# Performance work log

Measured on AMD Instinct MI355X. Metric: run time of the kernel, lower is better.

## Reference

```python
import jax, jax.numpy as jnp
import numpy as np

N_X, N_U, N_Y = 256, 32, 32
BATCH, T = 16, 8192
LAM_MIN, LAM_MAX = 0.9, 0.995
B_SCALE, D_SCALE = 0.25, 0.25


def setup_inputs() -> dict:
    key = jax.random.key(0)
    k = jax.random.split(key, 6)
    # Orthogonal Q via QR of a random Gaussian matrix (as in the torch module)
    M = jax.random.normal(k[0], (N_X, N_X), dtype=jnp.float32)
    Q, _ = jnp.linalg.qr(M)
    lam = LAM_MIN + (LAM_MAX - LAM_MIN) * jax.random.uniform(k[1], (N_X,), dtype=jnp.float32)
    Bmat = B_SCALE * jax.random.normal(k[2], (N_X, N_U), dtype=jnp.float32)
    # C picks out the first n_y coordinates (C[i, i] = 1)
    C = jnp.eye(N_Y, N_X, dtype=jnp.float32)
    D = D_SCALE * jax.random.normal(k[3], (N_Y, N_U), dtype=jnp.float32)
    x0 = jax.random.normal(k[4], (BATCH, N_X), dtype=jnp.float32)
    u = jax.random.normal(k[5], (BATCH, T, N_U), dtype=jnp.float32)
    return {"x0": x0, "u": u, "Q": Q, "lam": lam, "Bmat": Bmat, "C": C, "D": D}


def _diag_scan(lam, v):
    """Diagonal linear recurrence x_t = lam * x_{t-1} + v_t (x_0 folded into v[:, 0]).

    lam: (N,), v: (B, T, N) -> states x_1..x_T of shape (B, T, N).
    """
    a = jnp.broadcast_to(lam, v.shape)

    def op(l, r):
        a1, b1 = l
        a2, b2 = r
        return a1 * a2, a2 * b1 + b2

    return jax.lax.associative_scan(op, (a, v), axis=1)[1]


def reference(x0, u, Q, lam, Bmat, C, D):
    Bz = Q.T @ Bmat            # (n_x, n_u) modal input matrix
    Cz = C @ Q                 # (n_y, n_x) modal output matrix
    z0 = x0 @ Q                # (B, n_x)   modal initial state
    v = jnp.einsum('btu,nu->btn', u, Bz)   # (B, T, n_x)
    v = v.at[:, 0].add(lam * z0)            # fold lam * z0 into first step
    z_next = _diag_scan(lam, v)             # (B, T, n_x) = z_1..z_T
    # y_t uses z_t for t = 0..T-1 (states[:, :-1] in the original)
    z_prev = jnp.concatenate([z0[:, None, :], z_next[:, :-1]], axis=1)
    y = jnp.einsum('btn,yn->bty', z_prev, Cz) + jnp.einsum('btu,yu->bty', u, D)
    return y
```

## Files before the change

### kernel.cpp

```cpp
#include <hip/hip_runtime.h>

typedef _Float16 half4_t __attribute__((ext_vector_type(4)));
typedef _Float16 half8_t __attribute__((ext_vector_type(8)));
typedef float f32x4 __attribute__((ext_vector_type(4)));

constexpr int NX = 256, NU = 32, NY = 32, BATCH = 16, T = 8192;
constexpr int NC = 64, L = 128;
constexpr int SUBT = 32, NSUB = L / SUBT;
constexpr int ZP = 264;

__global__ __launch_bounds__(256) void k_pre(
    const float* __restrict__ x0, const float* __restrict__ Q,
    const float* __restrict__ Bm,
    _Float16* __restrict__ Bzh, float* __restrict__ z0)
{
    int o = blockIdx.x * 64 + (threadIdx.x >> 2);
    int p = threadIdx.x & 3;
    if (o >= 12288) return;
    float s = 0.f;
    int k0 = p * 64;
    if (o < 8192) {
        int n = o >> 5, j = o & 31;
        for (int k = k0; k < k0 + 64; ++k) s = fmaf(Q[k * NX + n], Bm[k * NU + j], s);
    } else {
        int g = o - 8192; int b = g >> 8, nn = g & 255;
        for (int k = k0; k < k0 + 64; ++k) s = fmaf(x0[b * NX + k], Q[k * NX + nn], s);
    }
    s += __shfl_xor(s, 1);
    s += __shfl_xor(s, 2);
    if (p == 0) {
        if (o < 8192) Bzh[o] = (_Float16)s;
        else          z0[o - 8192] = s;
    }
}

__global__ __launch_bounds__(256) void k_phase1(
    const float* __restrict__ u, const float* __restrict__ lam,
    const _Float16* __restrict__ Bzh, float* __restrict__ S)
{
    __shared__ __align__(16) _Float16 ut[2][SUBT][32];

    const int b = blockIdx.x >> 6, c = blockIdx.x & 63, tid = threadIdx.x;
    const int w = tid >> 6, lane = tid & 63, m16 = lane & 15, quad = lane >> 4;
    const int rot = (m16 & 3) * 8;
    const int tr = tid >> 3, cb = ((tid & 7) * 4 + (tr & 3) * 8) & 31;

    const float* ug = u + ((size_t)(b * T) + (size_t)c * L) * NU;
    float4 ucur = *(const float4*)(ug + tid * 4);

    half8_t bfrag[4];
    #pragma unroll
    for (int i = 0; i < 4; ++i)
        bfrag[i] = *(const half8_t*)&Bzh[((4 * w + i) * 16 + m16) * NU + quad * 8];

    float wr[4][4], wt16[4], l32[4], acc[4];
    #pragma unroll
    for (int i = 0; i < 4; ++i) {
        float la = lam[(4 * w + i) * 16 + m16];
        float p2 = la * la, p4 = p2 * p2, p8 = p4 * p4, p16 = p8 * p8;
        float inv1 = 1.0f / la;
        float inv4 = (inv1 * inv1) * (inv1 * inv1);
        float pq = 1.0f;
        if (quad & 1) pq *= inv4;
        if (quad & 2) pq *= inv4 * inv4;
        float w0 = (p16 * p8 * p4 * p2 * la) * pq;
        wr[i][0] = w0;
        wr[i][1] = w0 * inv1;
        wr[i][2] = wr[i][1] * inv1;
        wr[i][3] = wr[i][2] * inv1;
        wt16[i] = 1.0f / p16;
        l32[i] = p16 * p16;
        acc[i] = 0.f;
    }

    {
        half4_t h; h.x = (_Float16)ucur.x; h.y = (_Float16)ucur.y;
        h.z = (_Float16)ucur.z; h.w = (_Float16)ucur.w;
        *(half4_t*)&ut[0][tr][cb] = h;
    }
    __syncthreads();
    float4 unext = *(const float4*)(ug + (size_t)SUBT * NU + tid * 4);

    for (int sub = 0; sub < NSUB; ++sub) {
        half8_t af0 = *(const half8_t*)&ut[sub & 1][m16][(quad * 8 + rot) & 31];
        half8_t af1 = *(const half8_t*)&ut[sub & 1][16 + m16][(quad * 8 + rot) & 31];
        if (sub < NSUB - 2)
            ucur = *(const float4*)(ug + (size_t)(sub + 2) * SUBT * NU + tid * 4);
        #pragma unroll
        for (int i = 0; i < 4; ++i) {
            f32x4 z4 = {0.f, 0.f, 0.f, 0.f};
            f32x4 v0 = __builtin_amdgcn_mfma_f32_16x16x32_f16(af0, bfrag[i], z4, 0, 0, 0);
            f32x4 v1 = __builtin_amdgcn_mfma_f32_16x16x32_f16(af1, bfrag[i], z4, 0, 0, 0);
            float s0 = wr[i][0] * v0[0] + wr[i][1] * v0[1] + wr[i][2] * v0[2] + wr[i][3] * v0[3];
            float s1 = wr[i][0] * v1[0] + wr[i][1] * v1[1] + wr[i][2] * v1[2] + wr[i][3] * v1[3];
            acc[i] = fmaf(l32[i], acc[i], fmaf(wt16[i], s1, s0));
        }
        if (sub < NSUB - 1) {
            half4_t h; h.x = (_Float16)unext.x; h.y = (_Float16)unext.y;
            h.z = (_Float16)unext.z; h.w = (_Float16)unext.w;
            *(half4_t*)&ut[(sub + 1) & 1][tr][cb] = h;
            unext = ucur;
            __syncthreads();
        }
    }
    #pragma unroll
    for (int i = 0; i < 4; ++i) {
        acc[i] += __shfl_xor(acc[i], 16);
        acc[i] += __shfl_xor(acc[i], 32);
    }
    float out = quad == 0 ? acc[0] : quad == 1 ? acc[1] : quad == 2 ? acc[2] : acc[3];
    S[(size_t)blockIdx.x * NX + (4 * w + quad) * 16 + m16] = out;
}

__global__ __launch_bounds__(256) void k_phase3(
    const float* __restrict__ u, const float* __restrict__ lam,
    const _Float16* __restrict__ Bzh, const float* __restrict__ Q,
    const float* __restrict__ D, const float* __restrict__ S,
    const float* __restrict__ z0, float* __restrict__ y)
{
    __shared__ __align__(16) _Float16 ut[2][SUBT][32];
    __shared__ __align__(16) _Float16 zt[2][SUBT][ZP];
    __shared__ float pvec[NX];

    const int b = blockIdx.x >> 6, c = blockIdx.x & 63, tid = threadIdx.x;
    const int w = tid >> 6, lane = tid & 63, m16 = lane & 15, quad = lane >> 4;
    const int tw = w & 1, yw = w >> 1;
    const int rot = (m16 & 3) * 8;
    const int tr = tid >> 3, cb = ((tid & 7) * 4 + (tr & 3) * 8) & 31;

    const float* ug = u + ((size_t)(b * T) + (size_t)c * L) * NU;
    float4 ucur = *(const float4*)(ug + tid * 4);

    {
        float la = lam[tid];
        float l2L = 128.0f * __log2f(la);
        const float* Sb = S + (size_t)(b * NC) * NX + tid;
        float pv = 0.f;
        #pragma unroll 8
        for (int k = 0; k < c; ++k) {
            float wgt = exp2f((float)k * l2L);
            pv = fmaf(wgt, Sb[(size_t)(c - 1 - k) * NX], pv);
        }
        pvec[tid] = fmaf(exp2f((float)c * l2L), z0[b * NX + tid], pv);
    }

    half8_t bfrag[4];
    #pragma unroll
    for (int i = 0; i < 4; ++i)
        bfrag[i] = *(const half8_t*)&Bzh[((4 * w + i) * 16 + m16) * NU + quad * 8];
    half8_t wfrag[9];
    #pragma unroll
    for (int kk = 0; kk < 8; ++kk) {
        float4 qa = *(const float4*)&Q[(size_t)(yw * 16 + m16) * NX + kk * 32 + quad * 8];
        float4 qb = *(const float4*)&Q[(size_t)(yw * 16 + m16) * NX + kk * 32 + quad * 8 + 4];
        half8_t hh;
        hh[0] = (_Float16)qa.x; hh[1] = (_Float16)qa.y; hh[2] = (_Float16)qa.z; hh[3] = (_Float16)qa.w;
        hh[4] = (_Float16)qb.x; hh[5] = (_Float16)qb.y; hh[6] = (_Float16)qb.z; hh[7] = (_Float16)qb.w;
        wfrag[kk] = hh;
    }
    {
        float4 da = *(const float4*)&D[(size_t)(yw * 16 + m16) * NU + quad * 8];
        float4 db = *(const float4*)&D[(size_t)(yw * 16 + m16) * NU + quad * 8 + 4];
        half8_t hh;
        hh[0] = (_Float16)da.x; hh[1] = (_Float16)da.y; hh[2] = (_Float16)da.z; hh[3] = (_Float16)da.w;
        hh[4] = (_Float16)db.x; hh[5] = (_Float16)db.y; hh[6] = (_Float16)db.z; hh[7] = (_Float16)db.w;
        wfrag[8] = hh;
    }

    float lamn[4], inv1[4], iq[4], i16p[4], fq[4], f16p[4], l32[4], p[4];
    #pragma unroll
    for (int i = 0; i < 4; ++i) {
        int ni = (4 * w + i) * 16 + m16;
        float la = lam[ni];
        lamn[i] = la;
        float p2 = la * la, p4 = p2 * p2, p8 = p4 * p4, p16 = p8 * p8;
        float iv = 1.0f / la;
        inv1[i] = iv;
        float iv4 = (iv * iv) * (iv * iv);
        float pqi = 1.0f, pqf = 1.0f;
        if (quad & 1) { pqi *= iv4; pqf *= p4; }
        if (quad & 2) { pqi *= iv4 * iv4; pqf *= p8; }
        iq[i] = iv * pqi;
        fq[i] = pqf;
        i16p[i] = 1.0f / p16;
        f16p[i] = p16;
        l32[i] = p16 * p16;
    }

    {
        half4_t h; h.x = (_Float16)ucur.x; h.y = (_Float16)ucur.y;
        h.z = (_Float16)ucur.z; h.w = (_Float16)ucur.w;
        *(half4_t*)&ut[0][tr][cb] = h;
    }
    __syncthreads();
    #pragma unroll
    for (int i = 0; i < 4; ++i)
        p[i] = pvec[(4 * w + i) * 16 + m16];
    float4 unext = *(const float4*)(ug + (size_t)SUBT * NU + tid * 4);

    float* yg = y + ((size_t)(b * T) + (size_t)c * L) * NY;

    for (int sub = 0; sub < NSUB; ++sub) {
        half8_t af0 = *(const half8_t*)&ut[sub & 1][m16][(quad * 8 + rot) & 31];
        half8_t af1 = *(const half8_t*)&ut[sub & 1][16 + m16][(quad * 8 + rot) & 31];
        if (sub < NSUB - 2)
            ucur = *(const float4*)(ug + (size_t)(sub + 2) * SUBT * NU + tid * 4);
        #pragma unroll
        for (int i = 0; i < 4; ++i) {
            int ni = (4 * w + i) * 16 + m16;
            f32x4 z4 = {0.f, 0.f, 0.f, 0.f};
            f32x4 v0 = __builtin_amdgcn_mfma_f32_16x16x32_f16(af0, bfrag[i], z4, 0, 0, 0);
            f32x4 v1 = __builtin_amdgcn_mfma_f32_16x16x32_f16(af1, bfrag[i], z4, 0, 0, 0);
            float a0[4], a1[4];
            float sc = iq[i];
            #pragma unroll
            for (int r = 0; r < 4; ++r) {
                a0[r] = v0[r] * sc;
                a1[r] = v1[r] * (sc * i16p[i]);
                sc *= inv1[i];
            }
            float e0[4], e1[4];
            e0[0] = 0.f; e0[1] = a0[0]; e0[2] = e0[1] + a0[1]; e0[3] = e0[2] + a0[2];
            float S40 = e0[3] + a0[3];
            e1[0] = 0.f; e1[1] = a1[0]; e1[2] = e1[1] + a1[1]; e1[3] = e1[2] + a1[2];
            float S41 = e1[3] + a1[3];
            float incl0 = S40;
            float t0 = __shfl_up(incl0, 16); if (quad >= 1) incl0 += t0;
            t0 = __shfl_up(incl0, 32);       if (quad >= 2) incl0 += t0;
            float excl0 = incl0 - S40;
            float total0 = __shfl(incl0, 48 + m16);
            float incl1 = S41;
            float t1 = __shfl_up(incl1, 16); if (quad >= 1) incl1 += t1;
            t1 = __shfl_up(incl1, 32);       if (quad >= 2) incl1 += t1;
            float excl1 = incl1 - S41;
            float total1 = __shfl(incl1, 48 + m16);
            float f = fq[i];
            #pragma unroll
            for (int r = 0; r < 4; ++r) {
                float zv0 = f * (p[i] + (excl0 + e0[r]));
                float zv1 = (f * f16p[i]) * (p[i] + (total0 + excl1 + e1[r]));
                zt[sub & 1][quad * 4 + r][ni] = (_Float16)zv0;
                zt[sub & 1][16 + quad * 4 + r][ni] = (_Float16)zv1;
                f *= lamn[i];
            }
            p[i] = l32[i] * (p[i] + (total0 + total1));
        }
        if (sub < NSUB - 1) {
            half4_t h; h.x = (_Float16)unext.x; h.y = (_Float16)unext.y;
            h.z = (_Float16)unext.z; h.w = (_Float16)unext.w;
            *(half4_t*)&ut[(sub + 1) & 1][tr][cb] = h;
            unext = ucur;
        }
        __syncthreads();

        f32x4 acc = {0.f, 0.f, 0.f, 0.f};
        #pragma unroll
        for (int kk = 0; kk < 8; ++kk) {
            half8_t az = *(const half8_t*)&zt[sub & 1][tw * 16 + m16][kk * 32 + quad * 8];
            acc = __builtin_amdgcn_mfma_f32_16x16x32_f16(wfrag[kk], az, acc, 0, 0, 0);
        }
        {
            half8_t au = tw ? af1 : af0;
            acc = __builtin_amdgcn_mfma_f32_16x16x32_f16(wfrag[8], au, acc, 0, 0, 0);
        }
        {
            float4 v = make_float4(acc[0], acc[1], acc[2], acc[3]);
            *(float4*)&yg[(size_t)(sub * SUBT + tw * 16 + m16) * NY + yw * 16 + quad * 4] = v;
        }
    }
}

extern "C" void kernel_launch(void* const* d_in, const int* in_sizes, int n_in,
                              void* d_out, int out_size, void* d_ws, size_t ws_size,
                              hipStream_t stream) {
    (void)in_sizes; (void)n_in; (void)out_size; (void)ws_size;
    const float* x0  = (const float*)d_in[0];
    const float* u   = (const float*)d_in[1];
    const float* Q   = (const float*)d_in[2];
    const float* lam = (const float*)d_in[3];
    const float* Bm  = (const float*)d_in[4];
    const float* D   = (const float*)d_in[6];
    float* y = (float*)d_out;

    char* ws = (char*)d_ws;
    _Float16* Bzh = (_Float16*)(ws);
    float*    z0  = (float*)(ws + 16384);
    float*    S   = (float*)(ws + 32768);

    k_pre   <<<192, 256, 0, stream>>>(x0, Q, Bm, Bzh, z0);
    k_phase1<<<BATCH * NC, 256, 0, stream>>>(u, lam, Bzh, S);
    k_phase3<<<BATCH * NC, 256, 0, stream>>>(u, lam, Bzh, Q, D, S, z0, y);
}
```

Before: 118.4 us.

## Load MFMA input fragments directly from global memory, drop LDS staging of u

Each lane now reads its own u fragment rows from global memory, with a one-step register prefetch, and converts them to fp16 in registers. This replaces the cooperative load into LDS, the fp16 stores and the barrier per sub-tile. In phase3 the z tile goes from double buffering to a single buffer, with an extra barrier after the output MFMA to protect it, which cuts LDS use. In exchange, the u rows are read redundantly by every wave (4x in each block), and global loads are less coalesced than the earlier one-float4-per-thread pattern.

New measurement: 129.7 us. 9.5% more time.

```diff
diff --git a/kernel.cpp b/kernel.cpp
--- a/kernel.cpp
+++ b/kernel.cpp
@@ -8,6 +8,13 @@
 constexpr int NC = 64, L = 128;
 constexpr int SUBT = 32, NSUB = L / SUBT;
 constexpr int ZP = 264;
+
+__device__ __forceinline__ half8_t cvt8(float4 a, float4 b) {
+    half8_t h;
+    h[0] = (_Float16)a.x; h[1] = (_Float16)a.y; h[2] = (_Float16)a.z; h[3] = (_Float16)a.w;
+    h[4] = (_Float16)b.x; h[5] = (_Float16)b.y; h[6] = (_Float16)b.z; h[7] = (_Float16)b.w;
+    return h;
+}
 
 __global__ __launch_bounds__(256) void k_pre(
     const float* __restrict__ x0, const float* __restrict__ Q,
@@ -38,15 +45,15 @@
     const float* __restrict__ u, const float* __restrict__ lam,
     const _Float16* __restrict__ Bzh, float* __restrict__ S)
 {
-    __shared__ __align__(16) _Float16 ut[2][SUBT][32];
-
     const int b = blockIdx.x >> 6, c = blockIdx.x & 63, tid = threadIdx.x;
     const int w = tid >> 6, lane = tid & 63, m16 = lane & 15, quad = lane >> 4;
-    const int rot = (m16 & 3) * 8;
-    const int tr = tid >> 3, cb = ((tid & 7) * 4 + (tr & 3) * 8) & 31;
 
     const float* ug = u + ((size_t)(b * T) + (size_t)c * L) * NU;
-    float4 ucur = *(const float4*)(ug + tid * 4);
+    const float* r0 = ug + (size_t)m16 * NU + quad * 8;
+    const float* r1 = ug + (size_t)(16 + m16) * NU + quad * 8;
+
+    float4 c0a = *(const float4*)r0, c0b = *(const float4*)(r0 + 4);
+    float4 c1a = *(const float4*)r1, c1b = *(const float4*)(r1 + 4);
 
     half8_t bfrag[4];
     #pragma unroll
@@ -73,19 +80,15 @@
         acc[i] = 0.f;
     }
 
-    {
-        half4_t h; h.x = (_Float16)ucur.x; h.y = (_Float16)ucur.y;
-        h.z = (_Float16)ucur.z; h.w = (_Float16)ucur.w;
-        *(half4_t*)&ut[0][tr][cb] = h;
-    }
-    __syncthreads();
-    float4 unext = *(const float4*)(ug + (size_t)SUBT * NU + tid * 4);
-
     for (int sub = 0; sub < NSUB; ++sub) {
-        half8_t af0 = *(const half8_t*)&ut[sub & 1][m16][(quad * 8 + rot) & 31];
-        half8_t af1 = *(const half8_t*)&ut[sub & 1][16 + m16][(quad * 8 + rot) & 31];
-        if (sub < NSUB - 2)
-            ucur = *(const float4*)(ug + (size_t)(sub + 2) * SUBT * NU + tid * 4);
+        half8_t af0 = cvt8(c0a, c0b);
+        half8_t af1 = cvt8(c1a, c1b);
+        if (sub < NSUB - 1) {
+            const float* n0 = r0 + (size_t)(sub + 1) * SUBT * NU;
+            const float* n1 = r1 + (size_t)(sub + 1) * SUBT * NU;
+            c0a = *(const float4*)n0; c0b = *(const float4*)(n0 + 4);
+            c1a = *(const float4*)n1; c1b = *(const float4*)(n1 + 4);
+        }
         #pragma unroll
         for (int i = 0; i < 4; ++i) {
             f32x4 z4 = {0.f, 0.f, 0.f, 0.f};
@@ -95,13 +98,6 @@
             float s1 = wr[i][0] * v1[0] + wr[i][1] * v1[1] + wr[i][2] * v1[2] + wr[i][3] * v1[3];
             acc[i] = fmaf(l32[i], acc[i], fmaf(wt16[i], s1, s0));
         }
-        if (sub < NSUB - 1) {
-            half4_t h; h.x = (_Float16)unext.x; h.y = (_Float16)unext.y;
-            h.z = (_Float16)unext.z; h.w = (_Float16)unext.w;
-            *(half4_t*)&ut[(sub + 1) & 1][tr][cb] = h;
-            unext = ucur;
-            __syncthreads();
-        }
     }
     #pragma unroll
     for (int i = 0; i < 4; ++i) {
@@ -118,18 +114,19 @@
     const float* __restrict__ D, const float* __restrict__ S,
     const float* __restrict__ z0, float* __restrict__ y)
 {
-    __shared__ __align__(16) _Float16 ut[2][SUBT][32];
-    __shared__ __align__(16) _Float16 zt[2][SUBT][ZP];
+    __shared__ __align__(16) _Float16 zt[SUBT][ZP];
     __shared__ float pvec[NX];
 
     const int b = blockIdx.x >> 6, c = blockIdx.x & 63, tid = threadIdx.x;
     const int w = tid >> 6, lane = tid & 63, m16 = lane & 15, quad = lane >> 4;
     const int tw = w & 1, yw = w >> 1;
-    const int rot = (m16 & 3) * 8;
-    const int tr = tid >> 3, cb = ((tid & 7) * 4 + (tr & 3) * 8) & 31;
 
     const float* ug = u + ((size_t)(b * T) + (size_t)c * L) * NU;
-    float4 ucur = *(const float4*)(ug + tid * 4);
+    const float* r0 = ug + (size_t)m16 * NU + quad * 8;
+    const float* r1 = ug + (size_t)(16 + m16) * NU + quad * 8;
+
+    float4 c0a = *(const float4*)r0, c0b = *(const float4*)(r0 + 4);
+    float4 c1a = *(const float4*)r1, c1b = *(const float4*)(r1 + 4);
 
     {
         float la = lam[tid];
@@ -153,18 +150,12 @@
     for (int kk = 0; kk < 8; ++kk) {
         float4 qa = *(const float4*)&Q[(size_t)(yw * 16 + m16) * NX + kk * 32 + quad * 8];
         float4 qb = *(const float4*)&Q[(size_t)(yw * 16 + m16) * NX + kk * 32 + quad * 8 + 4];
-        half8_t hh;
-        hh[0] = (_Float16)qa.x; hh[1] = (_Float16)qa.y; hh[2] = (_Float16)qa.z; hh[3] = (_Float16)qa.w;
-        hh[4] = (_Float16)qb.x; hh[5] = (_Float16)qb.y; hh[6] = (_Float16)qb.z; hh[7] = (_Float16)qb.w;
-        wfrag[kk] = hh;
+        wfrag[kk] = cvt8(qa, qb);
     }
     {
         float4 da = *(const float4*)&D[(size_t)(yw * 16 + m16) * NU + quad * 8];
         float4 db = *(const float4*)&D[(size_t)(yw * 16 + m16) * NU + quad * 8 + 4];
-        half8_t hh;
-        hh[0] = (_Float16)da.x; hh[1] = (_Float16)da.y; hh[2] = (_Float16)da.z; hh[3] = (_Float16)da.w;
-        hh[4] = (_Float16)db.x; hh[5] = (_Float16)db.y; hh[6] = (_Float16)db.z; hh[7] = (_Float16)db.w;
-        wfrag[8] = hh;
+        wfrag[8] = cvt8(da, db);
     }
 
     float lamn[4], inv1[4], iq[4], i16p[4], fq[4], f16p[4], l32[4], p[4];
@@ -186,25 +177,22 @@
         f16p[i] = p16;
         l32[i] = p16 * p16;
     }
-
-    {
-        half4_t h; h.x = (_Float16)ucur.x; h.y = (_Float16)ucur.y;
-        h.z = (_Float16)ucur.z; h.w = (_Float16)ucur.w;
-        *(half4_t*)&ut[0][tr][cb] = h;
-    }
     __syncthreads();
     #pragma unroll
     for (int i = 0; i < 4; ++i)
         p[i] = pvec[(4 * w + i) * 16 + m16];
-    float4 unext = *(const float4*)(ug + (size_t)SUBT * NU + tid * 4);
 
     float* yg = y + ((size_t)(b * T) + (size_t)c * L) * NY;
 
     for (int sub = 0; sub < NSUB; ++sub) {
-        half8_t af0 = *(const half8_t*)&ut[sub & 1][m16][(quad * 8 + rot) & 31];
-        half8_t af1 = *(const half8_t*)&ut[sub & 1][16 + m16][(quad * 8 + rot) & 31];
-        if (sub < NSUB - 2)
-            ucur = *(const float4*)(ug + (size_t)(sub + 2) * SUBT * NU + tid * 4);
+        half8_t af0 = cvt8(c0a, c0b);
+        half8_t af1 = cvt8(c1a, c1b);
+        if (sub < NSUB - 1) {
+            const float* n0 = r0 + (size_t)(sub + 1) * SUBT * NU;
+            const float* n1 = r1 + (size_t)(sub + 1) * SUBT * NU;
+            c0a = *(const float4*)n0; c0b = *(const float4*)(n0 + 4);
+            c1a = *(const float4*)n1; c1b = *(const float4*)(n1 + 4);
+        }
         #pragma unroll
         for (int i = 0; i < 4; ++i) {
             int ni = (4 * w + i) * 16 + m16;
@@ -239,24 +227,18 @@
             for (int r = 0; r < 4; ++r) {
                 float zv0 = f * (p[i] + (excl0 + e0[r]));
                 float zv1 = (f * f16p[i]) * (p[i] + (total0 + excl1 + e1[r]));
-                zt[sub & 1][quad * 4 + r][ni] = (_Float16)zv0;
-                zt[sub & 1][16 + quad * 4 + r][ni] = (_Float16)zv1;
+                zt[quad * 4 + r][ni] = (_Float16)zv0;
+                zt[16 + quad * 4 + r][ni] = (_Float16)zv1;
                 f *= lamn[i];
             }
             p[i] = l32[i] * (p[i] + (total0 + total1));
         }
-        if (sub < NSUB - 1) {
-            half4_t h; h.x = (_Float16)unext.x; h.y = (_Float16)unext.y;
-            h.z = (_Float16)unext.z; h.w = (_Float16)unext.w;
-            *(half4_t*)&ut[(sub + 1) & 1][tr][cb] = h;
-            unext = ucur;
-        }
         __syncthreads();
 
         f32x4 acc = {0.f, 0.f, 0.f, 0.f};
         #pragma unroll
         for (int kk = 0; kk < 8; ++kk) {
-            half8_t az = *(const half8_t*)&zt[sub & 1][tw * 16 + m16][kk * 32 + quad * 8];
+            half8_t az = *(const half8_t*)&zt[tw * 16 + m16][kk * 32 + quad * 8];
             acc = __builtin_amdgcn_mfma_f32_16x16x32_f16(wfrag[kk], az, acc, 0, 0, 0);
         }
         {
@@ -267,6 +249,8 @@
             float4 v = make_float4(acc[0], acc[1], acc[2], acc[3]);
             *(float4*)&yg[(size_t)(sub * SUBT + tw * 16 + m16) * NY + yw * 16 + quad * 4] = v;
         }
+        if (sub < NSUB - 1)
+            __syncthreads();
     }
 }
 
```
